# Kernel tuning notes

Measured on AMD Instinct MI355X. Metric: run time of the kernel, lower is better.

Reference implementation:

```python
import jax, jax.numpy as jnp
import numpy as np

B, C, A = 4, 8, 9            # batch, num_classes, anchors per location
IMG = 512.0                   # image spatial size (square)
FEATS = [64, 32, 16, 8, 4]    # FPN feature map sizes
STRIDES = [8, 16, 32, 64, 128]
TOPK = 1000                   # topk_candidates_per_level
SCORE_THRESH = 0.05
NMS_THRESH = 0.5
DETS = 300                    # detections_per_img
BBOX_CLIP = float(np.log(1000.0 / 16.0))  # standard BoxCoder dw/dh clamp


def _make_anchors(f, stride):
    # 3 aspect ratios x 3 octave scales = 9 anchors per location (torchvision-style)
    base = stride * 4.0
    ratios = np.array([0.5, 1.0, 2.0])
    scales = np.array([2.0 ** 0, 2.0 ** (1.0 / 3.0), 2.0 ** (2.0 / 3.0)])
    ws, hs = [], []
    for r in ratios:
        for sc in scales:
            area = (base * sc) ** 2
            w = np.sqrt(area / r)
            ws.append(w)
            hs.append(w * r)
    ws = np.array(ws)
    hs = np.array(hs)
    shifts = (np.arange(f) + 0.5) * stride
    cx, cy = np.meshgrid(shifts, shifts, indexing='ij')  # H-major, matches map flatten
    cx = cx.reshape(-1)[:, None]
    cy = cy.reshape(-1)[:, None]
    boxes = np.stack([cx - ws / 2, cy - hs / 2, cx + ws / 2, cy + hs / 2], axis=-1)
    return boxes.reshape(-1, 4).astype(np.float32)  # [f*f*A, 4], location-major


def setup_inputs() -> dict:
    key = jax.random.key(0)
    inp = {}
    for i, (f, s) in enumerate(zip(FEATS, STRIDES)):
        k1 = jax.random.fold_in(key, 2 * i)
        k2 = jax.random.fold_in(key, 2 * i + 1)
        inp[f'cls_{i}'] = jax.random.normal(k1, (B, C * A, f, f), jnp.float32)
        inp[f'reg_{i}'] = 0.2 * jax.random.normal(k2, (B, 4 * A, f, f), jnp.float32)
        inp[f'anchors_{i}'] = jnp.asarray(_make_anchors(f, s))
    return inp


def _decode(reg, anc):
    # BoxCoder.decode with weights (1,1,1,1)
    aw = anc[..., 2] - anc[..., 0]
    ah = anc[..., 3] - anc[..., 1]
    acx = anc[..., 0] + 0.5 * aw
    acy = anc[..., 1] + 0.5 * ah
    dx, dy = reg[..., 0], reg[..., 1]
    dw = jnp.minimum(reg[..., 2], BBOX_CLIP)
    dh = jnp.minimum(reg[..., 3], BBOX_CLIP)
    pcx = dx * aw + acx
    pcy = dy * ah + acy
    pw = jnp.exp(dw) * aw
    ph = jnp.exp(dh) * ah
    boxes = jnp.stack([pcx - 0.5 * pw, pcy - 0.5 * ph, pcx + 0.5 * pw, pcy + 0.5 * ph], axis=-1)
    return jnp.clip(boxes, 0.0, IMG)  # clip_boxes_to_image


def _level_select(cls_map, reg_map, anchors):
    b, _, h, w = cls_map.shape
    # (B, A*C, H, W) -> (B, H*W*A, C) -> flat (B, H*W*A*C)
    logits = cls_map.reshape(b, A, C, h, w).transpose(0, 3, 4, 1, 2).reshape(b, -1)
    scores = jax.nn.sigmoid(logits)
    regs = reg_map.reshape(b, A, 4, h, w).transpose(0, 3, 4, 1, 2).reshape(b, -1, 4)
    top_s, top_i = jax.lax.top_k(scores, TOPK)  # topk_candidates_per_level
    anc_idx = top_i // C
    labels = top_i % C
    sel_reg = jnp.take_along_axis(regs, anc_idx[..., None], axis=1)  # [B,K,4]
    sel_anc = anchors[anc_idx]                                        # [B,K,4]
    boxes = _decode(sel_reg, sel_anc)
    top_s = jnp.where(top_s > SCORE_THRESH, top_s, -1.0)  # score threshold -> invalid
    return boxes, top_s, labels


def _pairwise_iou(a, b):
    lt = jnp.maximum(a[:, None, :2], b[None, :, :2])
    rb = jnp.minimum(a[:, None, 2:], b[None, :, 2:])
    wh = jnp.clip(rb - lt, 0.0)
    inter = wh[..., 0] * wh[..., 1]
    area_a = (a[:, 2] - a[:, 0]) * (a[:, 3] - a[:, 1])
    area_b = (b[:, 2] - b[:, 0]) * (b[:, 3] - b[:, 1])
    return inter / jnp.maximum(area_a[:, None] + area_b[None, :] - inter, 1e-7)


def _nms_image(boxes, scores, labels):
    # class-aware NMS via per-class coordinate offset (batched_nms trick)
    order = jnp.argsort(-scores)
    b = boxes[order]
    s = scores[order]
    l = labels[order]
    ob = b + (l.astype(b.dtype) * (IMG + 1.0))[:, None]
    iou = _pairwise_iou(jax.lax.stop_gradient(ob), jax.lax.stop_gradient(ob))
    n = s.shape[0]
    idxs = jnp.arange(n)
    def body(i, keep):
        sup = (iou[i] > NMS_THRESH) & keep[i] & (idxs > i)
        return keep & (~sup)
    keep = jax.lax.fori_loop(0, n, body, s > 0.0)
    s2 = jnp.where(keep, s, -1.0)
    top_s, idx = jax.lax.top_k(s2, DETS)  # detections_per_img
    valid = top_s > 0.0
    out_boxes = jnp.where(valid[:, None], b[idx], 0.0)
    out_scores = jnp.maximum(top_s, 0.0)
    out_labels = jnp.where(valid, l[idx], -1)
    return out_boxes, out_scores, out_labels


def reference(cls_0, cls_1, cls_2, cls_3, cls_4,
              reg_0, reg_1, reg_2, reg_3, reg_4,
              anchors_0, anchors_1, anchors_2, anchors_3, anchors_4):
    levels = [
        (cls_0, reg_0, anchors_0), (cls_1, reg_1, anchors_1),
        (cls_2, reg_2, anchors_2), (cls_3, reg_3, anchors_3),
        (cls_4, reg_4, anchors_4),
    ]
    outs = [_level_select(c, r, a) for c, r, a in levels]
    boxes = jnp.concatenate([o[0] for o in outs], axis=1)   # [B, 5*TOPK, 4]
    scores = jnp.concatenate([o[1] for o in outs], axis=1)  # [B, 5*TOPK]
    labels = jnp.concatenate([o[2] for o in outs], axis=1)
    return jax.vmap(_nms_image)(boxes, scores, labels)  # boxes [B,300,4], scores [B,300], labels [B,300]
```

## Files before the change

### kernel.cpp

```cpp
#include <hip/hip_runtime.h>
#include <stdint.h>
#include <stddef.h>

typedef unsigned int u32;
typedef unsigned long long u64;
typedef unsigned short u16;
typedef unsigned char u8;

#define NB 4
#define NLEV 5
#define NCH 72
#define NREGCH 36
#define TOPK 1000
#define NCAND 5000
#define NDET 300
#define NBINS 16384
#define RNB 4096
#define CAP 8192
#define FASTCAP 2048
#define CHUNK 8192
#define NCHUNK_IMG 50
#define DCH 512
#define DW 8
#define IMGSZ 512.0f
#define SCORE_TH 0.05f
#define NMS_TH 0.5f
#define BBOX_CLIP_F 4.135166556742356f

__constant__ int c_f[NLEV]    = {64, 32, 16, 8, 4};
__constant__ int c_Nloc[NLEV] = {4096, 1024, 256, 64, 16};
__constant__ int c_lg2[NLEV]  = {12, 10, 8, 6, 4};
__constant__ float c_tau[NLEV] = {2.594f, 2.075f, 1.433f, 0.513f, -1e30f};
__constant__ int c_rshift[NLEV] = {10, 10, 11, 12, 18};
__constant__ int c_nch[NLEV]  = {36, 9, 3, 1, 1};
__constant__ int c_clo[NLEV]  = {0, 36, 45, 48, 49};
__constant__ int c_ccap[NLEV] = {227, 910, 2730, 8192, 8192};

__device__ __forceinline__ float xla_tanh_f32(float x) {
  float ax = fabsf(x);
  float xc = fminf(fmaxf(x, -7.90531110763549805f), 7.90531110763549805f);
  float x2 = __fmul_rn(xc, xc);
  float p = -2.76076847742355e-16f;
  p = __fadd_rn(__fmul_rn(x2, p), 2.00018790482477e-13f);
  p = __fadd_rn(__fmul_rn(x2, p), -8.60467152213735e-11f);
  p = __fadd_rn(__fmul_rn(x2, p), 5.12229709037114e-08f);
  p = __fadd_rn(__fmul_rn(x2, p), 1.48572235717979e-05f);
  p = __fadd_rn(__fmul_rn(x2, p), 6.37261928875436e-04f);
  p = __fadd_rn(__fmul_rn(x2, p), 4.89352455891786e-03f);
  float num = __fmul_rn(xc, p);
  float q = 1.19825839466702e-06f;
  q = __fadd_rn(__fmul_rn(x2, q), 1.18534705686654e-04f);
  q = __fadd_rn(__fmul_rn(x2, q), 2.26843463243900e-03f);
  q = __fadd_rn(__fmul_rn(x2, q), 4.89352518554385e-03f);
  float r = __fdiv_rn(num, q);
  return (ax < 0.0004f) ? x : r;
}
__device__ __forceinline__ float sigmoid_ref(float x) {
  return __fadd_rn(0.5f, __fmul_rn(0.5f, xla_tanh_f32(__fmul_rn(0.5f, x))));
}

struct ClsPtrs { const float* p[NLEV]; };
struct LevelPtrs { const float* reg[NLEV]; const float* anc[NLEV]; };

__device__ __forceinline__ void chunk_map(int bid, int& b, int& level, int& chunk) {
  b = bid / NCHUNK_IMG;
  int cid = bid % NCHUNK_IMG;
  if      (cid < 36) { level = 0; chunk = cid; }
  else if (cid < 45) { level = 1; chunk = cid - 36; }
  else if (cid < 48) { level = 2; chunk = cid - 45; }
  else if (cid < 49) { level = 3; chunk = cid - 48; }
  else               { level = 4; chunk = cid - 49; }
}

__device__ __forceinline__ float4 decode_box(const LevelPtrs& lp, int b, int lv, u32 e) {
  u32 anc = e >> 3;
  int a = (int)(anc % 9u);
  int loc = (int)(anc / 9u);
  int f = c_f[lv];
  int Nloc = f * f;
  const float* rp = lp.reg[lv];
  const float* ap = lp.anc[lv] + (size_t)anc * 4;
  float r0 = rp[((size_t)b * NREGCH + (a * 4 + 0)) * Nloc + loc];
  float r1 = rp[((size_t)b * NREGCH + (a * 4 + 1)) * Nloc + loc];
  float r2 = rp[((size_t)b * NREGCH + (a * 4 + 2)) * Nloc + loc];
  float r3 = rp[((size_t)b * NREGCH + (a * 4 + 3)) * Nloc + loc];
  float a0 = ap[0], a1 = ap[1], a2 = ap[2], a3 = ap[3];
  float aw = __fsub_rn(a2, a0);
  float ah = __fsub_rn(a3, a1);
  float acx = __fadd_rn(a0, __fmul_rn(0.5f, aw));
  float acy = __fadd_rn(a1, __fmul_rn(0.5f, ah));
  float dw = fminf(r2, BBOX_CLIP_F);
  float dh = fminf(r3, BBOX_CLIP_F);
  float pcx = __fadd_rn(__fmul_rn(r0, aw), acx);
  float pcy = __fadd_rn(__fmul_rn(r1, ah), acy);
  float pw = __fmul_rn(expf(dw), aw);
  float ph = __fmul_rn(expf(dh), ah);
  float hx = __fmul_rn(0.5f, pw);
  float hy = __fmul_rn(0.5f, ph);
  float4 v;
  v.x = fminf(fmaxf(__fsub_rn(pcx, hx), 0.0f), IMGSZ);
  v.y = fminf(fmaxf(__fsub_rn(pcy, hy), 0.0f), IMGSZ);
  v.z = fminf(fmaxf(__fadd_rn(pcx, hx), 0.0f), IMGSZ);
  v.w = fminf(fmaxf(__fadd_rn(pcy, hy), 0.0f), IMGSZ);
  return v;
}

__global__ __launch_bounds__(256)
void k_filter(ClsPtrs cp, u32* __restrict__ bcnt, u64* __restrict__ sel) {
  int b, level, chunk;
  chunk_map(blockIdx.x, b, level, chunk);
  int Nloc = c_Nloc[level], lg2 = c_lg2[level];
  int Nsc = Nloc * NCH;
  int g = b * NLEV + level;
  const float* cls = cp.p[level] + (size_t)b * Nsc;
  float tau = c_tau[level];
  int base = chunk * CHUNK;
  int end = base + CHUNK; if (end > Nsc) end = Nsc;
  int wid = threadIdx.x >> 6, lane = threadIdx.x & 63;
  u64 lowm = (1ull << lane) - 1ull;
  __shared__ u32 wcnt[4];
  u32 mycnt = 0;
  for (int i = base + threadIdx.x; i < end; i += 256) {
    u64 mk = __ballot((int)(cls[i] > tau));
    mycnt += (u32)__popcll(mk);
  }
  if (lane == 0) wcnt[wid] = mycnt;
  __syncthreads();
  u32 wbase = 0, tot = 0;
  for (int w = 0; w < 4; ++w) { u32 c = wcnt[w]; if (w < wid) wbase += c; tot += c; }
  if (threadIdx.x == 0) bcnt[blockIdx.x] = tot;
  if (!tot) return;
  u32 ccap = (u32)c_ccap[level];
  size_t regbase = (size_t)g * CAP + (size_t)chunk * ccap;
  u32 run = 0;
  for (int i = base + threadIdx.x; i < end; i += 256) {
    float x = cls[i];
    bool selp = x > tau;
    u64 mk = __ballot((int)selp);
    if (selp) {
      u32 pos = wbase + run + (u32)__popcll(mk & lowm);
      if (pos < ccap) {
        u32 bits = __float_as_uint(sigmoid_ref(x));
        int ch = i >> lg2;
        int loc = i & (Nloc - 1);
        u32 e = (u32)(loc * NCH + ch);
        sel[regbase + pos] = ((u64)bits << 32) | (u32)(~e);
      }
    }
    run += (u32)__popcll(mk);
  }
}

__global__ __launch_bounds__(1024)
void k_rank(ClsPtrs cp, LevelPtrs lp, const u32* __restrict__ bcnt,
            const u64* __restrict__ sel,
            float* __restrict__ cand_s, u32* __restrict__ cand_t,
            float4* __restrict__ cand_box) {
  __shared__ union {
    struct { u64 keysC[FASTCAP]; u64 keys2[FASTCAP]; u32 hist[RNB]; u32 pfx[RNB]; } f;
    u32 histfb[NBINS];
    u64 keysfb[CAP];
  } sh;
  __shared__ u32 part[1024];
  __shared__ u32 ccnt[36];
  __shared__ u32 cbase[37];
  __shared__ u32 s_ovf;
  __shared__ u32 s_last;
  __shared__ u32 s_cnt;
  __shared__ int s_cut;
  int g = blockIdx.x;
  int b = g / NLEV, l = g % NLEV;
  int Nloc = c_Nloc[l], lg2 = c_lg2[l];
  int Nsc = Nloc * NCH;
  int tid = threadIdx.x;
  int lane = tid & 63;
  u64 lowm = (1ull << lane) - 1ull;
  int obase = b * NCAND + l * TOPK;
  int nch = c_nch[l], clo = c_clo[l];
  u32 ccap = (u32)c_ccap[l];
  if (tid < nch) ccnt[tid] = bcnt[b * NCHUNK_IMG + clo + tid];
  __syncthreads();
  if (tid == 0) {
    u32 a = 0, ovf = 0;
    for (int c = 0; c < nch; ++c) { cbase[c] = a; a += ccnt[c]; if (ccnt[c] > ccap) ovf = 1; }
    cbase[nch] = a; s_ovf = ovf;
  }
  __syncthreads();
  u32 cnt = cbase[nch];
  bool fast = (cnt >= TOPK) && (cnt <= FASTCAP) && !s_ovf;
  if (fast) {
    u32 m = cnt;
    int shift = c_rshift[l];
    for (int c = 0; c < nch; ++c) {
      u32 cc = ccnt[c], cb2 = cbase[c];
      for (u32 i = tid; i < cc; i += 1024)
        sh.f.keysC[cb2 + i] = sel[(size_t)g * CAP + (size_t)c * ccap + i];
    }
    for (int i = tid; i < RNB; i += 1024) sh.f.hist[i] = 0;
    if (tid == 0) s_last = 0;
    __syncthreads();
    u64 k0a = ((u32)tid < m)        ? sh.f.keysC[tid]        : 0ULL;
    u64 k0b = ((u32)tid + 1024 < m) ? sh.f.keysC[tid + 1024] : 0ULL;
    auto bkt_of = [&](u64 k) -> int {
      int d = (int)0x3F800000 - (int)(u32)(k >> 32);
      if (d < 0) d = 0;
      int bq = d >> shift;
      return bq > RNB - 1 ? RNB - 1 : bq;
    };
    int ba = bkt_of(k0a), bb = bkt_of(k0b);
    if ((u32)tid < m)        atomicAdd(&sh.f.hist[ba], 1u);
    if ((u32)tid + 1024 < m) atomicAdd(&sh.f.hist[bb], 1u);
    __syncthreads();
    {
      int t4 = tid * 4;
      u32 h0 = sh.f.hist[t4], h1 = sh.f.hist[t4 + 1], h2 = sh.f.hist[t4 + 2], h3 = sh.f.hist[t4 + 3];
      u32 s4 = h0 + h1 + h2 + h3;
      u32 x = s4;
      for (int d = 1; d < 64; d <<= 1) { u32 y = __shfl_up(x, d); if (lane >= d) x += y; }
      if (lane == 63) part[tid >> 6] = x;
      __syncthreads();
      if (tid == 0) { u32 a = 0; for (int w = 0; w < 16; ++w) { u32 c = part[w]; part[w] = a; a += c; } }
      __syncthreads();
      u32 base2 = part[tid >> 6] + (x - s4);
      sh.f.pfx[t4]     = base2;
      sh.f.pfx[t4 + 1] = base2 + h0;
      sh.f.pfx[t4 + 2] = base2 + h0 + h1;
      sh.f.pfx[t4 + 3] = base2 + h0 + h1 + h2;
    }
    __syncthreads();
    if ((u32)tid < m)        { u32 p = atomicAdd(&sh.f.pfx[ba], 1u); sh.f.keys2[p] = k0a; }
    if ((u32)tid + 1024 < m) { u32 p = atomicAdd(&sh.f.pfx[bb], 1u); sh.f.keys2[p] = k0b; }
    __syncthreads();
    auto emit = [&](u64 k0, int bkt) {
      u32 endq = sh.f.pfx[bkt];
      u32 startq = endq - sh.f.hist[bkt];
      u32 r = startq;
      for (u32 j = startq; j < endq; ++j) r += (sh.f.keys2[j] > k0) ? 1u : 0u;
      if (r < TOPK) {
        u32 hi = (u32)(k0 >> 32);
        cand_s[obase + r] = __uint_as_float(hi);
        u32 e = ~((u32)k0);
        cand_t[obase + r] = ((u32)l << 19) | (e & 0x7FFFFu);
        cand_box[obase + r] = decode_box(lp, b, l, e);
        if (r == TOPK - 1) s_last = hi;
      }
    };
    if ((u32)tid < m)        emit(k0a, ba);
    if ((u32)tid + 1024 < m) emit(k0b, bb);
    __syncthreads();
    u32 bits_tau = __float_as_uint(sigmoid_ref(c_tau[l]));
    if ((int)cnt != Nsc && !(s_last > bits_tau + 64u)) fast = false;
  }
  if (fast) return;

  const float* cls = cp.p[l] + (size_t)b * Nsc;
  __syncthreads();
  for (int i = tid; i < NBINS; i += 1024) sh.histfb[i] = 0;
  if (tid == 0) s_cnt = 0;
  __syncthreads();
  for (int i = tid; i < Nsc; i += 1024) {
    float s = sigmoid_ref(cls[i]);
    atomicAdd(&sh.histfb[__float_as_uint(s) >> 16], 1u);
  }
  __syncthreads();
  { u32 a = 0; for (int j = 0; j < 16; ++j) a += sh.histfb[tid * 16 + j]; part[tid] = a; }
  __syncthreads();
  if (tid == 0) {
    u32 cum = 0; int cut = 0;
    for (int ch = 1023; ch >= 0; --ch) {
      if (cum + part[ch] >= TOPK) {
        u32 cc = cum;
        for (int bin = ch * 16 + 15;; --bin) { cc += sh.histfb[bin]; if (cc >= TOPK) { cut = bin; break; } }
        break;
      }
      cum += part[ch];
    }
    s_cut = cut;
  }
  __syncthreads();
  int cut = s_cut;
  __syncthreads();
  for (int i = tid; i < Nsc; i += 1024) {
    float s = sigmoid_ref(cls[i]);
    u32 bits = __float_as_uint(s);
    bool selp = (int)(bits >> 16) >= cut;
    u64 mk = __ballot((int)selp);
    if (selp) {
      int ldr = __builtin_ctzll(mk);
      u32 pos0 = 0;
      if (lane == ldr) pos0 = atomicAdd(&s_cnt, (u32)__popcll(mk));
      pos0 = (u32)__shfl((int)pos0, ldr);
      u32 pos = pos0 + (u32)__popcll(mk & lowm);
      if (pos < CAP) {
        int ch = i >> lg2;
        int loc = i & (Nloc - 1);
        u32 e = (u32)(loc * NCH + ch);
        sh.keysfb[pos] = ((u64)bits << 32) | (u32)(~e);
      }
    }
  }
  __syncthreads();
  u32 m2 = s_cnt; if (m2 > CAP) m2 = CAP;
  for (u32 i = tid; i < m2; i += 1024) {
    u64 k0 = sh.keysfb[i];
    u32 r = 0;
    #pragma unroll 8
    for (u32 j = 0; j < m2; ++j) r += (sh.keysfb[j] > k0) ? 1u : 0u;
    if (r < TOPK) {
      cand_s[obase + r] = __uint_as_float((u32)(k0 >> 32));
      u32 e = ~((u32)k0);
      cand_t[obase + r] = ((u32)l << 19) | (e & 0x7FFFFu);
      cand_box[obase + r] = decode_box(lp, b, l, e);
    }
  }
  for (u32 r = m2 + tid; r < TOPK; r += 1024) {
    cand_s[obase + r] = -1.0f;
    cand_t[obase + r] = ((u32)l << 19) | r;
    cand_box[obase + r] = make_float4(0.f, 0.f, 0.f, 0.f);
  }
}

__global__ __launch_bounds__(1024)
void k_grank(const float* __restrict__ cand_s, const u32* __restrict__ cand_t,
             const float4* __restrict__ cand_box,
             float4* __restrict__ rboxOff, u32* __restrict__ rmeta) {
  __shared__ u64 keys[NCAND];
  __shared__ int vc[NLEV];
  int b = blockIdx.y;
  int seg = blockIdx.x;
  int tid = threadIdx.x;
  for (int i = tid; i < NCAND; i += 1024) {
    float s = cand_s[b * NCAND + i];
    u32 t = cand_t[b * NCAND + i];
    u32 hi = (s > SCORE_TH) ? __float_as_uint(s) : 0u;
    keys[i] = ((u64)hi << 32) | (u32)(~t);
  }
  __syncthreads();
  if (tid < NLEV) {
    const u64* A = keys + tid * TOPK;
    int lo = 0, h2 = TOPK;
    while (lo < h2) { int mid = (lo + h2) >> 1; if (A[mid] >> 32) lo = mid + 1; else h2 = mid; }
    vc[tid] = lo;
  }
  __syncthreads();
  if (tid >= TOPK) return;
  int i = seg * TOPK + tid;
  u64 k0 = keys[i];
  u32 hi = (u32)(k0 >> 32);
  u32 t = ~((u32)k0);
  int rank;
  u32 cls = 0;
  if (hi) {
    rank = tid;
    for (int L = 0; L < NLEV; ++L) {
      if (L == seg) continue;
      const u64* A = keys + L * TOPK;
      int lo = 0, h2 = TOPK;
      while (lo < h2) { int mid = (lo + h2) >> 1; if (A[mid] > k0) lo = mid + 1; else h2 = mid; }
      rank += lo;
    }
    cls = t & 7u;
  } else {
    int tv = 0, before = 0;
    for (int L = 0; L < NLEV; ++L) { tv += vc[L]; if (L < seg) before += TOPK - vc[L]; }
    rank = tv + before + (tid - vc[seg]);
  }
  float4 v = cand_box[b * NCAND + i];
  float off = __fmul_rn((float)cls, IMGSZ + 1.0f);
  float4 q;
  q.x = __fadd_rn(v.x, off); q.y = __fadd_rn(v.y, off);
  q.z = __fadd_rn(v.z, off); q.w = __fadd_rn(v.w, off);
  rboxOff[b * NCAND + rank] = q;
  rmeta[b * NCAND + rank] = hi ? (((u32)i << 8) | cls) : 0xFFFFFFFFu;
}

__device__ __forceinline__ bool iou_gt4(float4 p, float pa, float4 q, float qa) {
  float ltx = fmaxf(p.x, q.x), lty = fmaxf(p.y, q.y);
  float rx  = fminf(p.z, q.z), ry  = fminf(p.w, q.w);
  float ww = fmaxf(__fsub_rn(rx, ltx), 0.0f);
  float hh = fmaxf(__fsub_rn(ry, lty), 0.0f);
  float inter = __fmul_rn(ww, hh);
  bool res = false;
  if (inter > 0.0f) {
    float denom = fmaxf(__fsub_rn(__fadd_rn(pa, qa), inter), 1e-7f);
    res = __fdiv_rn(inter, denom) > NMS_TH;
  }
  return res;
}
__device__ __forceinline__ float area_rn(float4 p) {
  return __fmul_rn(__fsub_rn(p.z, p.x), __fsub_rn(p.w, p.y));
}

__global__ __launch_bounds__(256)
void k_mask(const float4* __restrict__ rboxOff, u64* __restrict__ rowsG) {
  __shared__ float4 sb[DCH];
  __shared__ float  sa[DCH];
  int b = blockIdx.y, rb = blockIdx.x;
  int tid = threadIdx.x;
  for (int i = tid; i < DCH; i += 256) {
    float4 q = rboxOff[b * NCAND + i];
    sb[i] = q; sa[i] = area_rn(q);
  }
  __syncthreads();
  int lane = tid & 63, wv = tid >> 6;
  int r = rb * 64 + lane;
  float4 qr = sb[r]; float ar = sa[r];
  u64* rowp = rowsG + ((size_t)b * DCH + r) * DW;
  for (int w = wv; w < rb; w += 4) rowp[w] = 0;
  for (int w = rb + wv; w < DW; w += 4) {
    u64 bits = 0;
    int j0 = w * 64;
    if (w > rb) {
      #pragma unroll 4
      for (int jc = 0; jc < 64; ++jc)
        if (iou_gt4(qr, ar, sb[j0 + jc], sa[j0 + jc])) bits |= 1ull << jc;
    } else {
      #pragma unroll 4
      for (int jc = 0; jc < 64; ++jc) {
        int j = j0 + jc;
        if (j > r && iou_gt4(qr, ar, sb[j], sa[j])) bits |= 1ull << jc;
      }
    }
    rowp[w] = bits;
  }
}

__global__ __launch_bounds__(1024)
void k_detect(const float* __restrict__ cand_s, const float4* __restrict__ cand_box,
              const float4* __restrict__ rboxOff, const u32* __restrict__ rmeta,
              const u64* __restrict__ rowsG, float* __restrict__ out) {
  __shared__ u64 rows[DCH][DW];
  __shared__ u32 sm[DCH];
  __shared__ u32 nzmap[DCH / 32];
  __shared__ u64 validm[DW], keptm[DW];
  __shared__ float4 kbox[NDET];
  __shared__ float  karea2[NDET];
  __shared__ u32    kmeta[NDET];
  __shared__ float4 cbox[64];
  __shared__ float  carea[64];
  __shared__ u64    supsh[16];
  __shared__ u32 s_nk, s_stop;
  int b = blockIdx.x, tid = threadIdx.x;
  int lane = tid & 63, wid = tid >> 6;
  if (tid < DCH / 32) nzmap[tid] = 0;
  if (tid == 0) { s_nk = 0; s_stop = 0; }
  __syncthreads();
  for (int k = tid; k < DCH * DW; k += 1024) {
    u64 v = rowsG[(size_t)b * DCH * DW + k];
    ((u64*)rows)[k] = v;
    if (v) atomicOr(&nzmap[(k / DW) >> 5], 1u << ((k / DW) & 31));
  }
  if (tid < DCH) sm[tid] = rmeta[b * NCAND + tid];
  __syncthreads();
  if (tid < DCH) {
    u64 bv = __ballot((int)(sm[tid] != 0xFFFFFFFFu));
    if (lane == 0) validm[tid >> 6] = bv;
  }
  __syncthreads();
  if (tid == 0) {
    u64 kw[DW];
    #pragma unroll
    for (int w = 0; w < DW; ++w) kw[w] = validm[w];
    for (int mw = 0; mw < DCH / 32; ++mw) {
      u32 nzw = nzmap[mw];
      while (nzw) {
        int bit = __builtin_ctz(nzw); nzw &= nzw - 1;
        int i = mw * 32 + bit;
        if ((kw[i >> 6] >> (i & 63)) & 1ull) {
          #pragma unroll
          for (int v = 0; v < DW; ++v) kw[v] &= ~rows[i][v];
        }
      }
    }
    #pragma unroll
    for (int w = 0; w < DW; ++w) keptm[w] = kw[w];
  }
  __syncthreads();
  if (tid < DCH) {
    int w = tid >> 6;
    u64 kwv = keptm[w];
    if ((kwv >> (tid & 63)) & 1ull) {
      u32 pre = 0;
      for (int v = 0; v < w; ++v) pre += (u32)__popcll(keptm[v]);
      pre += (u32)__popcll(kwv & ((1ull << (tid & 63)) - 1ull));
      if (pre < NDET) {
        float4 q = rboxOff[b * NCAND + tid];
        kbox[pre] = q; karea2[pre] = area_rn(q); kmeta[pre] = sm[tid];
      }
    }
  }
  __syncthreads();
  if (tid == 0) {
    u32 add = 0, nvalid = 0;
    #pragma unroll
    for (int w = 0; w < DW; ++w) { add += (u32)__popcll(keptm[w]); nvalid += (u32)__popcll(validm[w]); }
    u32 nn = add; if (nn > NDET) nn = NDET;
    s_nk = nn;
    if (nn >= (u32)NDET || nvalid < (u32)DCH) s_stop = 1;
  }
  __syncthreads();

  int n = (int)s_nk;
  for (int base = DCH; base < NCAND && !s_stop; base += 64) {
    int ci = base + lane;
    u32 meta = (ci < NCAND) ? rmeta[b * NCAND + ci] : 0xFFFFFFFFu;
    bool valid = meta != 0xFFFFFFFFu;
    float4 q = (ci < NCAND) ? rboxOff[b * NCAND + ci] : make_float4(0.f, 0.f, 0.f, 0.f);
    float aq = area_rn(q);
    if (wid == 0) { cbox[lane] = q; carea[lane] = aq; }
    bool sup = false;
    if (valid) for (int k = wid; k < n; k += 16) sup = sup | iou_gt4(kbox[k], karea2[k], q, aq);
    u64 bal = __ballot((int)sup);
    if (lane == 0) supsh[wid] = bal;
    __syncthreads();
    if (wid == 0) {
      u64 supm = 0;
      for (int w = 0; w < 16; ++w) supm |= supsh[w];
      u64 vm = __ballot((int)valid);
      u64 pending = vm & ~supm;
      u64 row = 0;
      if ((pending >> lane) & 1ull) {
        u64 mine = pending & ~((2ull << lane) - 1ull);
        while (mine) {
          int j = __builtin_ctzll(mine); mine &= mine - 1ull;
          if (iou_gt4(q, aq, cbox[j], carea[j])) row |= (1ull << j);
        }
      }
      __shared__ u64 rowsh2[64];
      rowsh2[lane] = row;
      u64 nz = __ballot((int)(row != 0ull));
      bool done = false;
      u64 rem = pending;
      while (rem) {
        int r = __builtin_ctzll(rem); rem &= rem - 1ull;
        if (lane == r) { kmeta[n] = meta; kbox[n] = q; karea2[n] = aq; }
        ++n;
        if (n == NDET) { done = true; break; }
        if ((nz >> r) & 1ull) rem &= ~rowsh2[r];
      }
      if (__any((int)(!valid))) done = true;
      if (lane == 0) { s_nk = (u32)n; s_stop = done ? 1u : 0u; }
    }
    __syncthreads();
    n = (int)s_nk;
  }

  int nf = (int)s_nk;
  for (int k = tid; k < NDET; k += 1024) {
    float bx0 = 0.f, bx1 = 0.f, bx2 = 0.f, bx3 = 0.f, sc = 0.f, lb = -1.0f;
    if (k < nf) {
      u32 m = kmeta[k];
      int io = (int)(m >> 8);
      float4 v = cand_box[b * NCAND + io];
      bx0 = v.x; bx1 = v.y; bx2 = v.z; bx3 = v.w;
      sc = cand_s[b * NCAND + io];
      lb = (float)(m & 0xFFu);
    }
    int idx = b * NDET + k;
    out[(size_t)idx * 4 + 0] = bx0;
    out[(size_t)idx * 4 + 1] = bx1;
    out[(size_t)idx * 4 + 2] = bx2;
    out[(size_t)idx * 4 + 3] = bx3;
    out[NB * NDET * 4 + idx] = sc;
    out[NB * NDET * 5 + idx] = lb;
  }
}

extern "C" void kernel_launch(void* const* d_in, const int* in_sizes, int n_in,
                              void* d_out, int out_size, void* d_ws, size_t ws_size,
                              hipStream_t stream) {
  const float* cls[NLEV]; const float* reg[NLEV]; const float* anc[NLEV];
  bool dict_order = (n_in >= 2) && (in_sizes[1] == 4 * NREGCH * 64 * 64);
  for (int l = 0; l < NLEV; ++l) {
    if (dict_order) {
      cls[l] = (const float*)d_in[3 * l + 0];
      reg[l] = (const float*)d_in[3 * l + 1];
      anc[l] = (const float*)d_in[3 * l + 2];
    } else {
      cls[l] = (const float*)d_in[l];
      reg[l] = (const float*)d_in[NLEV + l];
      anc[l] = (const float*)d_in[2 * NLEV + l];
    }
  }

  char* ws = (char*)d_ws;
  size_t off = 0;
  auto alloc = [&](size_t bytes) -> void* {
    void* p = ws + off;
    off = (off + bytes + 255) & ~(size_t)255;
    return p;
  };
  u32*    bcnt     = (u32*)   alloc((size_t)NB * NCHUNK_IMG * 4);
  u64*    sel      = (u64*)   alloc(20ULL * CAP * 8);
  float*  cand_s   = (float*) alloc((size_t)NB * NCAND * 4);
  u32*    cand_t   = (u32*)   alloc((size_t)NB * NCAND * 4);
  float4* cand_box = (float4*)alloc((size_t)NB * NCAND * 16);
  float4* rboxOff  = (float4*)alloc((size_t)NB * NCAND * 16);
  u32*    rmeta    = (u32*)   alloc((size_t)NB * NCAND * 4);
  u64*    rowsG    = (u64*)   alloc((size_t)NB * DCH * DW * 8);
  (void)ws_size; (void)out_size;

  ClsPtrs cp;
  for (int l = 0; l < NLEV; ++l) cp.p[l] = cls[l];
  LevelPtrs lp;
  for (int l = 0; l < NLEV; ++l) { lp.reg[l] = reg[l]; lp.anc[l] = anc[l]; }

  k_filter<<<NB * NCHUNK_IMG, 256, 0, stream>>>(cp, bcnt, sel);
  k_rank<<<NB * NLEV, 1024, 0, stream>>>(cp, lp, bcnt, sel, cand_s, cand_t, cand_box);
  k_grank<<<dim3(NLEV, NB), 1024, 0, stream>>>(cand_s, cand_t, cand_box, rboxOff, rmeta);
  k_mask<<<dim3(DW, NB), 256, 0, stream>>>(rboxOff, rowsG);
  k_detect<<<NB, 1024, 0, stream>>>(cand_s, cand_box, rboxOff, rmeta, rowsG, (float*)d_out);
}
```

Baseline: 69.96 us.

## Fuse global rank, IoU mask and detect kernels into one per-image kernel

Merges k_grank, k_mask and k_detect into a single kernel launched with one 1024-thread block per image. The first 512 ranked boxes stay in shared memory, and the suppression mask lives in shared memory through a union with the key array, so the global round trips through rboxOff/rowsG for those boxes and two kernel launches go away. In exchange, parallelism drops from 20 and 32 blocks to 4 blocks for the rank and mask stages. Separately, the chunk gather in k_rank now uses one flat loop with a binary search over chunk bases instead of a loop per chunk.

```diff
diff --git a/kernel.cpp b/kernel.cpp
--- a/kernel.cpp
+++ b/kernel.cpp
@@ -191,10 +191,10 @@
   if (fast) {
     u32 m = cnt;
     int shift = c_rshift[l];
-    for (int c = 0; c < nch; ++c) {
-      u32 cc = ccnt[c], cb2 = cbase[c];
-      for (u32 i = tid; i < cc; i += 1024)
-        sh.f.keysC[cb2 + i] = sel[(size_t)g * CAP + (size_t)c * ccap + i];
+    for (u32 i = tid; i < m; i += 1024) {
+      int lo = 0, h2 = nch - 1;
+      while (lo < h2) { int mid = (lo + h2 + 1) >> 1; if (cbase[mid] <= i) lo = mid; else h2 = mid - 1; }
+      sh.f.keysC[i] = sel[(size_t)g * CAP + (size_t)lo * ccap + (i - cbase[lo])];
     }
     for (int i = tid; i < RNB; i += 1024) sh.f.hist[i] = 0;
     if (tid == 0) s_last = 0;
@@ -320,60 +320,6 @@
   }
 }
 
-__global__ __launch_bounds__(1024)
-void k_grank(const float* __restrict__ cand_s, const u32* __restrict__ cand_t,
-             const float4* __restrict__ cand_box,
-             float4* __restrict__ rboxOff, u32* __restrict__ rmeta) {
-  __shared__ u64 keys[NCAND];
-  __shared__ int vc[NLEV];
-  int b = blockIdx.y;
-  int seg = blockIdx.x;
-  int tid = threadIdx.x;
-  for (int i = tid; i < NCAND; i += 1024) {
-    float s = cand_s[b * NCAND + i];
-    u32 t = cand_t[b * NCAND + i];
-    u32 hi = (s > SCORE_TH) ? __float_as_uint(s) : 0u;
-    keys[i] = ((u64)hi << 32) | (u32)(~t);
-  }
-  __syncthreads();
-  if (tid < NLEV) {
-    const u64* A = keys + tid * TOPK;
-    int lo = 0, h2 = TOPK;
-    while (lo < h2) { int mid = (lo + h2) >> 1; if (A[mid] >> 32) lo = mid + 1; else h2 = mid; }
-    vc[tid] = lo;
-  }
-  __syncthreads();
-  if (tid >= TOPK) return;
-  int i = seg * TOPK + tid;
-  u64 k0 = keys[i];
-  u32 hi = (u32)(k0 >> 32);
-  u32 t = ~((u32)k0);
-  int rank;
-  u32 cls = 0;
-  if (hi) {
-    rank = tid;
-    for (int L = 0; L < NLEV; ++L) {
-      if (L == seg) continue;
-      const u64* A = keys + L * TOPK;
-      int lo = 0, h2 = TOPK;
-      while (lo < h2) { int mid = (lo + h2) >> 1; if (A[mid] > k0) lo = mid + 1; else h2 = mid; }
-      rank += lo;
-    }
-    cls = t & 7u;
-  } else {
-    int tv = 0, before = 0;
-    for (int L = 0; L < NLEV; ++L) { tv += vc[L]; if (L < seg) before += TOPK - vc[L]; }
-    rank = tv + before + (tid - vc[seg]);
-  }
-  float4 v = cand_box[b * NCAND + i];
-  float off = __fmul_rn((float)cls, IMGSZ + 1.0f);
-  float4 q;
-  q.x = __fadd_rn(v.x, off); q.y = __fadd_rn(v.y, off);
-  q.z = __fadd_rn(v.z, off); q.w = __fadd_rn(v.w, off);
-  rboxOff[b * NCAND + rank] = q;
-  rmeta[b * NCAND + rank] = hi ? (((u32)i << 8) | cls) : 0xFFFFFFFFu;
-}
-
 __device__ __forceinline__ bool iou_gt4(float4 p, float pa, float4 q, float qa) {
   float ltx = fmaxf(p.x, q.x), lty = fmaxf(p.y, q.y);
   float rx  = fminf(p.z, q.z), ry  = fminf(p.w, q.w);
@@ -391,67 +337,112 @@
   return __fmul_rn(__fsub_rn(p.z, p.x), __fsub_rn(p.w, p.y));
 }
 
-__global__ __launch_bounds__(256)
-void k_mask(const float4* __restrict__ rboxOff, u64* __restrict__ rowsG) {
+__global__ __launch_bounds__(1024)
+void k_fused(const float* __restrict__ cand_s, const u32* __restrict__ cand_t,
+             const float4* __restrict__ cand_box,
+             float4* __restrict__ rboxOff, u32* __restrict__ rmeta,
+             float* __restrict__ out) {
+  __shared__ union {
+    u64 keys[NCAND];
+    u64 rows[DCH][DW];
+  } u;
   __shared__ float4 sb[DCH];
   __shared__ float  sa[DCH];
-  int b = blockIdx.y, rb = blockIdx.x;
-  int tid = threadIdx.x;
-  for (int i = tid; i < DCH; i += 256) {
-    float4 q = rboxOff[b * NCAND + i];
-    sb[i] = q; sa[i] = area_rn(q);
-  }
-  __syncthreads();
-  int lane = tid & 63, wv = tid >> 6;
-  int r = rb * 64 + lane;
-  float4 qr = sb[r]; float ar = sa[r];
-  u64* rowp = rowsG + ((size_t)b * DCH + r) * DW;
-  for (int w = wv; w < rb; w += 4) rowp[w] = 0;
-  for (int w = rb + wv; w < DW; w += 4) {
-    u64 bits = 0;
-    int j0 = w * 64;
-    if (w > rb) {
-      #pragma unroll 4
-      for (int jc = 0; jc < 64; ++jc)
-        if (iou_gt4(qr, ar, sb[j0 + jc], sa[j0 + jc])) bits |= 1ull << jc;
-    } else {
-      #pragma unroll 4
-      for (int jc = 0; jc < 64; ++jc) {
-        int j = j0 + jc;
-        if (j > r && iou_gt4(qr, ar, sb[j], sa[j])) bits |= 1ull << jc;
-      }
-    }
-    rowp[w] = bits;
-  }
-}
-
-__global__ __launch_bounds__(1024)
-void k_detect(const float* __restrict__ cand_s, const float4* __restrict__ cand_box,
-              const float4* __restrict__ rboxOff, const u32* __restrict__ rmeta,
-              const u64* __restrict__ rowsG, float* __restrict__ out) {
-  __shared__ u64 rows[DCH][DW];
-  __shared__ u32 sm[DCH];
-  __shared__ u32 nzmap[DCH / 32];
-  __shared__ u64 validm[DW], keptm[DW];
+  __shared__ u32    sm[DCH];
+  __shared__ int    vc[NLEV];
+  __shared__ u32    nzmap[DCH / 32];
+  __shared__ u64    validm[DW], keptm[DW];
   __shared__ float4 kbox[NDET];
   __shared__ float  karea2[NDET];
   __shared__ u32    kmeta[NDET];
   __shared__ float4 cbox[64];
   __shared__ float  carea[64];
   __shared__ u64    supsh[16];
-  __shared__ u32 s_nk, s_stop;
+  __shared__ u64    rowsh2[64];
+  __shared__ u32    s_nk, s_stop;
   int b = blockIdx.x, tid = threadIdx.x;
   int lane = tid & 63, wid = tid >> 6;
+
+  for (int i = tid; i < NCAND; i += 1024) {
+    float s = cand_s[b * NCAND + i];
+    u32 t = cand_t[b * NCAND + i];
+    u32 hi = (s > SCORE_TH) ? __float_as_uint(s) : 0u;
+    u.keys[i] = ((u64)hi << 32) | (u32)(~t);
+  }
   if (tid < DCH / 32) nzmap[tid] = 0;
   if (tid == 0) { s_nk = 0; s_stop = 0; }
   __syncthreads();
-  for (int k = tid; k < DCH * DW; k += 1024) {
-    u64 v = rowsG[(size_t)b * DCH * DW + k];
-    ((u64*)rows)[k] = v;
-    if (v) atomicOr(&nzmap[(k / DW) >> 5], 1u << ((k / DW) & 31));
-  }
-  if (tid < DCH) sm[tid] = rmeta[b * NCAND + tid];
-  __syncthreads();
+  if (tid < NLEV) {
+    const u64* A = u.keys + tid * TOPK;
+    int lo = 0, h2 = TOPK;
+    while (lo < h2) { int mid = (lo + h2) >> 1; if (A[mid] >> 32) lo = mid + 1; else h2 = mid; }
+    vc[tid] = lo;
+  }
+  __syncthreads();
+  for (int k5 = 0; k5 < 5; ++k5) {
+    int i = tid + k5 * 1024;
+    if (i >= NCAND) break;
+    u64 k0 = u.keys[i];
+    u32 hi = (u32)(k0 >> 32);
+    u32 t = ~((u32)k0);
+    int seg = i / TOPK;
+    int rank;
+    u32 cls = 0;
+    if (hi) {
+      rank = i - seg * TOPK;
+      for (int L = 0; L < NLEV; ++L) {
+        if (L == seg) continue;
+        const u64* A = u.keys + L * TOPK;
+        int lo = 0, h2 = TOPK;
+        while (lo < h2) { int mid = (lo + h2) >> 1; if (A[mid] > k0) lo = mid + 1; else h2 = mid; }
+        rank += lo;
+      }
+      cls = t & 7u;
+    } else {
+      int tv = 0, before = 0;
+      for (int L = 0; L < NLEV; ++L) { tv += vc[L]; if (L < seg) before += TOPK - vc[L]; }
+      rank = tv + before + ((i - seg * TOPK) - vc[seg]);
+    }
+    float4 v = cand_box[b * NCAND + i];
+    float off = __fmul_rn((float)cls, IMGSZ + 1.0f);
+    float4 q;
+    q.x = __fadd_rn(v.x, off); q.y = __fadd_rn(v.y, off);
+    q.z = __fadd_rn(v.z, off); q.w = __fadd_rn(v.w, off);
+    u32 meta = hi ? (((u32)i << 8) | cls) : 0xFFFFFFFFu;
+    if (rank < DCH) {
+      sb[rank] = q; sa[rank] = area_rn(q); sm[rank] = meta;
+    } else {
+      rboxOff[b * NCAND + rank] = q;
+      rmeta[b * NCAND + rank] = meta;
+    }
+  }
+  __syncthreads();
+  {
+    int rb = wid >> 1, half = wid & 1;
+    int r = rb * 64 + lane;
+    float4 qr = sb[r]; float ar = sa[r];
+    bool any = false;
+    for (int w = half; w < DW; w += 2) {
+      u64 bits = 0;
+      if (w >= rb) {
+        int j0 = w * 64;
+        if (w > rb) {
+          #pragma unroll 4
+          for (int jc = 0; jc < 64; ++jc)
+            if (iou_gt4(qr, ar, sb[j0 + jc], sa[j0 + jc])) bits |= 1ull << jc;
+        } else {
+          #pragma unroll 4
+          for (int jc = 0; jc < 64; ++jc) {
+            int j = j0 + jc;
+            if (j > r && iou_gt4(qr, ar, sb[j], sa[j])) bits |= 1ull << jc;
+          }
+        }
+      }
+      u.rows[r][w] = bits;
+      any |= (bits != 0);
+    }
+    if (any) atomicOr(&nzmap[r >> 5], 1u << (r & 31));
+  }
   if (tid < DCH) {
     u64 bv = __ballot((int)(sm[tid] != 0xFFFFFFFFu));
     if (lane == 0) validm[tid >> 6] = bv;
@@ -468,7 +459,7 @@
         int i = mw * 32 + bit;
         if ((kw[i >> 6] >> (i & 63)) & 1ull) {
           #pragma unroll
-          for (int v = 0; v < DW; ++v) kw[v] &= ~rows[i][v];
+          for (int v = 0; v < DW; ++v) kw[v] &= ~u.rows[i][v];
         }
       }
     }
@@ -483,10 +474,7 @@
       u32 pre = 0;
       for (int v = 0; v < w; ++v) pre += (u32)__popcll(keptm[v]);
       pre += (u32)__popcll(kwv & ((1ull << (tid & 63)) - 1ull));
-      if (pre < NDET) {
-        float4 q = rboxOff[b * NCAND + tid];
-        kbox[pre] = q; karea2[pre] = area_rn(q); kmeta[pre] = sm[tid];
-      }
+      if (pre < NDET) { kbox[pre] = sb[tid]; karea2[pre] = sa[tid]; kmeta[pre] = sm[tid]; }
     }
   }
   __syncthreads();
@@ -526,7 +514,6 @@
           if (iou_gt4(q, aq, cbox[j], carea[j])) row |= (1ull << j);
         }
       }
-      __shared__ u64 rowsh2[64];
       rowsh2[lane] = row;
       u64 nz = __ballot((int)(row != 0ull));
       bool done = false;
@@ -597,7 +584,6 @@
   float4* cand_box = (float4*)alloc((size_t)NB * NCAND * 16);
   float4* rboxOff  = (float4*)alloc((size_t)NB * NCAND * 16);
   u32*    rmeta    = (u32*)   alloc((size_t)NB * NCAND * 4);
-  u64*    rowsG    = (u64*)   alloc((size_t)NB * DCH * DW * 8);
   (void)ws_size; (void)out_size;
 
   ClsPtrs cp;
@@ -607,7 +593,5 @@
 
   k_filter<<<NB * NCHUNK_IMG, 256, 0, stream>>>(cp, bcnt, sel);
   k_rank<<<NB * NLEV, 1024, 0, stream>>>(cp, lp, bcnt, sel, cand_s, cand_t, cand_box);
-  k_grank<<<dim3(NLEV, NB), 1024, 0, stream>>>(cand_s, cand_t, cand_box, rboxOff, rmeta);
-  k_mask<<<dim3(DW, NB), 256, 0, stream>>>(rboxOff, rowsG);
-  k_detect<<<NB, 1024, 0, stream>>>(cand_s, cand_box, rboxOff, rmeta, rowsG, (float*)d_out);
-}
+  k_fused<<<NB, 1024, 0, stream>>>(cand_s, cand_t, cand_box, rboxOff, rmeta, (float*)d_out);
+}
```

After: 81.16 us. 16.0% more time.
